# Kernel optimization log

Measured on AMD Instinct MI355X. Metric: run time of the kernel, lower is better.

The kernel has to match this reference:

```python
import jax, jax.numpy as jnp
import numpy as np

D_MODEL = 2048
NUM_HEADS = 16
N_KV_HEADS = 4
HEAD_DIM = D_MODEL // NUM_HEADS  # 128
N_REP = NUM_HEADS // N_KV_HEADS  # 4
WINDOW = 256
ROPE_BASE = 10000.0
B, T = 2, 2048


def setup_inputs() -> dict:
    key = jax.random.key(0)
    ks = jax.random.split(key, 5)
    s_in = 1.0 / np.sqrt(D_MODEL)
    return {
        "x": jax.random.normal(ks[0], (B, T, D_MODEL), jnp.float32),
        "Wq": jax.random.normal(ks[1], (D_MODEL, D_MODEL), jnp.float32) * s_in,
        "Wk": jax.random.normal(ks[2], (D_MODEL, N_KV_HEADS * HEAD_DIM), jnp.float32) * s_in,
        "Wv": jax.random.normal(ks[3], (D_MODEL, N_KV_HEADS * HEAD_DIM), jnp.float32) * s_in,
        "Wo": jax.random.normal(ks[4], (D_MODEL, D_MODEL), jnp.float32) * s_in,
    }


def _rope_tables(seqlen, dtype):
    inv_freq = 1.0 / (ROPE_BASE ** (jnp.arange(0, HEAD_DIM, 2, dtype=jnp.float32) / HEAD_DIM))
    t = jnp.arange(seqlen, dtype=jnp.float32)
    freqs = jnp.outer(t, inv_freq)              # [T, hd/2]
    emb = jnp.concatenate([freqs, freqs], -1)   # [T, hd]
    return jnp.cos(emb).astype(dtype), jnp.sin(emb).astype(dtype)


def _rotate_half(x):
    half = x.shape[-1] // 2
    return jnp.concatenate([-x[..., half:], x[..., :half]], -1)


def reference(x, Wq, Wk, Wv, Wo):
    Bb, Tt, _ = x.shape
    q = (x @ Wq).reshape(Bb, Tt, NUM_HEADS, HEAD_DIM).transpose(0, 2, 1, 3)   # [B,H,T,hd]
    k = (x @ Wk).reshape(Bb, Tt, N_KV_HEADS, HEAD_DIM).transpose(0, 2, 1, 3)  # [B,Hkv,T,hd]
    v = (x @ Wv).reshape(Bb, Tt, N_KV_HEADS, HEAD_DIM).transpose(0, 2, 1, 3)

    cos, sin = _rope_tables(Tt, q.dtype)  # [T, hd] each, broadcast over B,H
    q = q * cos + _rotate_half(q) * sin
    k = k * cos + _rotate_half(k) * sin

    # GQA: repeat kv heads to match query heads
    k = jnp.repeat(k, N_REP, axis=1)
    v = jnp.repeat(v, N_REP, axis=1)

    # banded causal sliding-window mask: 0 <= i - j < WINDOW
    rel = jnp.arange(Tt)[:, None] - jnp.arange(Tt)[None, :]
    allowed = (rel >= 0) & (rel < WINDOW)  # [T, T]

    scale = 1.0 / np.sqrt(HEAD_DIM)
    scores = jnp.einsum('bhqd,bhkd->bhqk', q, k) * scale
    scores = jnp.where(allowed, scores, jnp.finfo(scores.dtype).min)
    probs = jax.nn.softmax(scores, axis=-1)
    y = jnp.einsum('bhqk,bhkd->bhqd', probs, v)
    y = y.transpose(0, 2, 1, 3).reshape(Bb, Tt, D_MODEL)
    return y @ Wo
```

## Files before the change

### kernel.cpp

```cpp
#include <hip/hip_runtime.h>
#include <hip/hip_bf16.h>

#define D_MODEL 2048
#define SEQ_T   2048
#define NQH     16
#define NKVH    4
#define HD      128
#define WIN     256
#define BATCH   2
#define ROWS    (BATCH * SEQ_T)
#define L2_10K  13.287712379549449f
#define GK      2048

typedef __attribute__((ext_vector_type(8))) short bf8_t;
typedef __attribute__((ext_vector_type(4))) float f4_t;

__device__ __forceinline__ float bf2f(unsigned short u) {
    union { unsigned int i; float f; } v; v.i = ((unsigned int)u) << 16; return v.f;
}
__device__ __forceinline__ unsigned short f2bf(float f) {
    union { float f; unsigned int i; } v; v.f = f;
    unsigned int x = v.i;
    unsigned int lsb = (x >> 16) & 1u;
    x += 0x7fffu + lsb;
    return (unsigned short)(x >> 16);
}

__device__ __forceinline__ void async_ld16(const unsigned short* g, unsigned short* l) {
    __builtin_amdgcn_global_load_lds(
        (const __attribute__((address_space(1))) unsigned int*)(g),
        (__attribute__((address_space(3))) unsigned int*)(l), 16, 0, 0);
}

__device__ int sniff_is_f32(const unsigned short* p) {
    int sane = 0;
    for (int i = 0; i < 64; ++i) {
        unsigned short u = p[2 * i];
        int e = (u >> 7) & 0xFF;
        sane += (e >= 100 && e <= 140) ? 1 : 0;
    }
    return sane < 32;
}

__global__ __launch_bounds__(256)
void convert_all(const float* __restrict__ x,
                 const float* __restrict__ Wq, const float* __restrict__ Wk,
                 const float* __restrict__ Wv, const float* __restrict__ Wo,
                 unsigned short* __restrict__ xb,
                 unsigned short* __restrict__ Wqkvt, unsigned short* __restrict__ Wot) {
    __shared__ unsigned short Ts[32][36];
    int id = blockIdx.x;
    const int t = threadIdx.x;
    if (id < 4096) {
        int i = (id * 256 + t) * 8;
        float4 a = *(const float4*)(x + i);
        float4 b = *(const float4*)(x + i + 4);
        ushort4 o0, o1;
        o0.x = f2bf(a.x); o0.y = f2bf(a.y); o0.z = f2bf(a.z); o0.w = f2bf(a.w);
        o1.x = f2bf(b.x); o1.y = f2bf(b.y); o1.z = f2bf(b.z); o1.w = f2bf(b.w);
        *(ushort4*)(xb + i)     = o0;
        *(ushort4*)(xb + i + 4) = o1;
        return;
    }
    id -= 4096;
    const float* W; unsigned short* Wt; int N;
    const int K = D_MODEL;
    if (id < 4096)      { W = Wq; Wt = Wqkvt;                          N = 2048; }
    else if (id < 5120) { W = Wk; Wt = Wqkvt + (size_t)2048 * D_MODEL; N = 512;  id -= 4096; }
    else if (id < 6144) { W = Wv; Wt = Wqkvt + (size_t)2560 * D_MODEL; N = 512;  id -= 5120; }
    else                { W = Wo; Wt = Wot;                            N = 2048; id -= 6144; }
    const int ntn = N >> 5;
    const int n0 = (id % ntn) * 32;
    const int k0 = (id / ntn) * 32;
    {
        int r = t >> 3, c = (t & 7) * 4;
        float4 v = *(const float4*)(W + (size_t)(k0 + r) * N + n0 + c);
        Ts[r][c + 0] = f2bf(v.x); Ts[r][c + 1] = f2bf(v.y);
        Ts[r][c + 2] = f2bf(v.z); Ts[r][c + 3] = f2bf(v.w);
    }
    __syncthreads();
    {
        int n = t >> 3, k = (t & 7) * 4;
        ushort4 o;
        o.x = Ts[k + 0][n]; o.y = Ts[k + 1][n];
        o.z = Ts[k + 2][n]; o.w = Ts[k + 3][n];
        *(ushort4*)(Wt + (size_t)(n0 + n) * K + k0 + k) = o;
    }
}

__global__ __launch_bounds__(256, 3)
void gemm128r(const unsigned short* __restrict__ A,
              const unsigned short* __restrict__ Bt,
              void* __restrict__ Cq, void* __restrict__ Ck, void* __restrict__ Cvc,
              int N, int mode) {
    __shared__ __align__(16) unsigned short Ls[3][8192];

    const int tid  = threadIdx.x;
    const int w    = tid >> 6;
    const int lane = tid & 63;
    const int quad = lane >> 4;
    const int lr   = lane & 15;
    const int wm   = w >> 1;
    const int wn   = w & 1;
    const int sl   = ((quad + (lr >> 1)) & 3) * 8;

    const int ntn = N >> 7;
    const int g   = blockIdx.x;
    const int xcd = g & 7;
    const int r   = g >> 3;
    const int bm  = (xcd & 3) * 8 + (r & 7);
    const int bn  = (xcd >> 2) * (ntn >> 1) + (r >> 3);
    const int m0  = bm * 128;
    const int n0  = bn * 128;

    const unsigned short* srcA[2];
    const unsigned short* srcB[2];
    int dchunk[2];
    #pragma unroll
    for (int l = 0; l < 2; ++l) {
        int li   = l * 256 + tid;
        int row  = li >> 2;
        int slog = ((li & 3) - ((li >> 3) & 3)) & 3;
        srcA[l]   = A  + (size_t)(m0 + row) * GK + slog * 8;
        srcB[l]   = Bt + (size_t)(n0 + row) * GK + slog * 8;
        dchunk[l] = (l * 256 + w * 64) * 8;
    }

    f4_t acc[4][4];
    #pragma unroll
    for (int i = 0; i < 4; ++i)
        #pragma unroll
        for (int j = 0; j < 4; ++j) acc[i][j] = (f4_t){0.f, 0.f, 0.f, 0.f};

#define STAGE(S, KT) do {                                           \
        const int ko_ = (KT) * 32;                                  \
        async_ld16(srcA[0] + ko_, &Ls[S][dchunk[0]]);               \
        async_ld16(srcA[1] + ko_, &Ls[S][dchunk[1]]);               \
        async_ld16(srcB[0] + ko_, &Ls[S][4096 + dchunk[0]]);        \
        async_ld16(srcB[1] + ko_, &Ls[S][4096 + dchunk[1]]);        \
    } while (0)

#define GATE(NN) asm volatile("s_waitcnt vmcnt(" #NN ")" ::: "memory")

    STAGE(0, 0); STAGE(1, 1);
    GATE(4);
    __builtin_amdgcn_s_barrier();

    int Sc = 0, Ss = 2;
    for (int t = 0; t < 64; ++t) {
        const unsigned short* LA = &Ls[Sc][0];
        const unsigned short* LB = &Ls[Sc][4096];
        bf8_t af[4], bv[4];
        #pragma unroll
        for (int mf = 0; mf < 4; ++mf)
            af[mf] = *(const bf8_t*)&LA[(wm * 64 + mf * 16 + lr) * 32 + sl];
        #pragma unroll
        for (int nf = 0; nf < 4; ++nf)
            bv[nf] = *(const bf8_t*)&LB[(wn * 16 + nf * 32 + lr) * 32 + sl];
        if (t < 62) STAGE(Ss, t + 2);
        __builtin_amdgcn_s_setprio(1);
        #pragma unroll
        for (int nf = 0; nf < 4; ++nf)
            #pragma unroll
            for (int mf = 0; mf < 4; ++mf)
                acc[mf][nf] = __builtin_amdgcn_mfma_f32_16x16x32_bf16(
                    af[mf], bv[nf], acc[mf][nf], 0, 0, 0);
        __builtin_amdgcn_s_setprio(0);
        if (t < 62)       GATE(4);
        else if (t == 62) GATE(0);
        if (t < 63) __builtin_amdgcn_s_barrier();
        Sc = (Sc == 2) ? 0 : Sc + 1;
        Ss = (Ss == 2) ? 0 : Ss + 1;
    }

#undef STAGE
#undef GATE

    if (mode == 1) {
        float* C = (float*)Cq;
        #pragma unroll
        for (int mf = 0; mf < 4; ++mf)
            #pragma unroll
            for (int nf = 0; nf < 4; ++nf) {
                int c  = n0 + wn * 16 + nf * 32 + lr;
                int rb = m0 + wm * 64 + mf * 16 + quad * 4;
                #pragma unroll
                for (int rr = 0; rr < 4; ++rr)
                    C[(size_t)(rb + rr) * N + c] = acc[mf][nf][rr];
            }
        return;
    }
    if (n0 < 2048 + 512) {
        const bool isQ = (n0 < 2048);
        unsigned short* Cb = isQ ? (unsigned short*)Cq : (unsigned short*)Ck;
        const int ldc = isQ ? D_MODEL : (NKVH * HD);
        const int cb0 = isQ ? n0 : (n0 - 2048);
        float inv[2];
        #pragma unroll
        for (int p = 0; p < 2; ++p)
            inv[p] = exp2f(-(float)(wn * 16 + p * 32 + lr) * (L2_10K / 64.0f));
        #pragma unroll
        for (int mf = 0; mf < 4; ++mf) {
            #pragma unroll
            for (int rr = 0; rr < 4; ++rr) {
                int row = m0 + wm * 64 + mf * 16 + quad * 4 + rr;
                float tp = (float)(row & (SEQ_T - 1));
                #pragma unroll
                for (int p = 0; p < 2; ++p) {
                    float sn, cs;
                    sincosf(tp * inv[p], &sn, &cs);
                    float lo = acc[mf][p][rr], hi = acc[mf][p + 2][rr];
                    size_t base = (size_t)row * ldc + cb0 + wn * 16 + p * 32 + lr;
                    Cb[base]      = f2bf(lo * cs - hi * sn);
                    Cb[base + 64] = f2bf(hi * cs + lo * sn);
                }
            }
        }
    } else {
        unsigned short* Vc = (unsigned short*)Cvc;
        #pragma unroll
        for (int mf = 0; mf < 4; ++mf)
            #pragma unroll
            for (int nf = 0; nf < 4; ++nf) {
                int n    = (n0 - 2560) + wn * 16 + nf * 32 + lr;
                int kvh2 = n >> 7, d = n & 127;
                int row0 = m0 + wm * 64 + mf * 16 + quad * 4;
                int bb   = row0 >> 11, pos = row0 & (SEQ_T - 1);
                ushort4 o;
                o.x = f2bf(acc[mf][nf][0]); o.y = f2bf(acc[mf][nf][1]);
                o.z = f2bf(acc[mf][nf][2]); o.w = f2bf(acc[mf][nf][3]);
                *(ushort4*)(Vc + (size_t)(bb * 4 + kvh2) * (SEQ_T * HD)
                              + (size_t)(pos >> 5) * 4096 + d * 32 + (pos & 31)) = o;
            }
    }
}

__global__ __launch_bounds__(512, 2)
void gemm128(const unsigned short* __restrict__ A,
             const unsigned short* __restrict__ Bt,
             float* __restrict__ C, int N) {
    __shared__ __align__(16) unsigned short Ls[4][12288];

    const int tid  = threadIdx.x;
    const int w    = tid >> 6;
    const int lane = tid & 63;
    const int quad = lane >> 4;
    const int lr   = lane & 15;
    const int wm   = w >> 2;
    const int wn   = w & 3;
    const int sl   = ((quad + (lr >> 1)) & 3) * 8;

    const int ntn = N >> 8;
    const int g   = blockIdx.x;
    const int xcd = g & 7;
    const int r   = g >> 3;
    const int bm  = (xcd & 3) * 8 + (r & 7);
    const int bn  = (xcd >> 2) * (ntn >> 1) + (r >> 3);
    const int m0  = bm * 128;
    const int n0  = bn * 256;

    const int slog = ((tid & 3) - ((tid >> 3) & 3)) & 3;
    const unsigned short* srcA0 = A  + (size_t)(m0 + (tid >> 2)) * GK + slog * 8;
    const unsigned short* srcB0 = Bt + (size_t)(n0 + (tid >> 2)) * GK + slog * 8;
    const unsigned short* srcB1 = Bt + (size_t)(n0 + 128 + (tid >> 2)) * GK + slog * 8;
    const int dch = w * 512;

    f4_t acc[4][4];
    #pragma unroll
    for (int i = 0; i < 4; ++i)
        #pragma unroll
        for (int j = 0; j < 4; ++j) acc[i][j] = (f4_t){0.f, 0.f, 0.f, 0.f};

#define STAGEB(S, KT) do {                                          \
        const int ko_ = (KT) * 32;                                  \
        async_ld16(srcA0 + ko_, &Ls[S][dch]);                       \
        async_ld16(srcB0 + ko_, &Ls[S][4096 + dch]);                \
        async_ld16(srcB1 + ko_, &Ls[S][8192 + dch]);                \
    } while (0)

#define GATE(NN) asm volatile("s_waitcnt vmcnt(" #NN ")" ::: "memory")

    STAGEB(0, 0); STAGEB(1, 1); STAGEB(2, 2);
    GATE(6);
    __builtin_amdgcn_s_barrier();

    bf8_t af[4], bv[4];
    for (int t = 0; t < 64; ++t) {
        const int S = t & 3;
        #pragma unroll
        for (int mf = 0; mf < 4; ++mf)
            af[mf] = *(const bf8_t*)&Ls[S][(wm * 64 + mf * 16 + lr) * 32 + sl];
        #pragma unroll
        for (int nf = 0; nf < 4; ++nf)
            bv[nf] = *(const bf8_t*)&Ls[S][4096 + (wn * 16 + nf * 64 + lr) * 32 + sl];
        if (t < 61) STAGEB((t + 3) & 3, t + 3);
        __builtin_amdgcn_s_barrier();
        __builtin_amdgcn_s_setprio(1);
        #pragma unroll
        for (int nf = 0; nf < 4; ++nf)
            #pragma unroll
            for (int mf = 0; mf < 4; ++mf)
                acc[mf][nf] = __builtin_amdgcn_mfma_f32_16x16x32_bf16(
                    af[mf], bv[nf], acc[mf][nf], 0, 0, 0);
        __builtin_amdgcn_s_setprio(0);
        if (t < 61)      GATE(6);
        else if (t == 61) GATE(3);
        else if (t == 62) GATE(0);
        if (t < 63) __builtin_amdgcn_s_barrier();
    }

#undef STAGEB
#undef GATE

    #pragma unroll
    for (int mf = 0; mf < 4; ++mf)
        #pragma unroll
        for (int nf = 0; nf < 4; ++nf) {
            int c  = n0 + wn * 16 + nf * 64 + lr;
            int rb = m0 + wm * 64 + mf * 16 + quad * 4;
            #pragma unroll
            for (int rr = 0; rr < 4; ++rr)
                C[(size_t)(rb + rr) * N + c] = acc[mf][nf][rr];
        }
}

__global__ __launch_bounds__(256)
void gemm_dual(const void* __restrict__ A, const void* __restrict__ B,
               void* __restrict__ C, int M, int N, int Kd,
               const unsigned short* __restrict__ sniffp,
               int a_dyn, int c_dyn, int c_trans) {
    __shared__ unsigned short As[64][32];
    __shared__ unsigned short Bs[64][32];
    __shared__ int s_f32;

    const int t = threadIdx.x;
    if (t == 0) s_f32 = sniff_is_f32(sniffp);

    const int m0 = blockIdx.y * 64, n0 = blockIdx.x * 64;
    const int w = t >> 6, lane = t & 63;
    const int wm = w >> 1, wn = w & 1;
    const int quad = lane >> 4, lr = lane & 15;

    f4_t acc[2][2];
    #pragma unroll
    for (int i = 0; i < 2; ++i)
        #pragma unroll
        for (int j = 0; j < 2; ++j)
            acc[i][j] = (f4_t){0.f, 0.f, 0.f, 0.f};

    const int ar = t >> 2, ac = (t & 3) * 8;
    const int bk = t >> 3, bn = (t & 7) * 8;

    __syncthreads();
    const bool in_f32 = (s_f32 != 0);
    const bool a_f32  = in_f32 && (a_dyn != 0);
    const bool c_f32  = in_f32 && (c_dyn != 0);

    for (int k0 = 0; k0 < Kd; k0 += 32) {
        __syncthreads();
        if (a_f32) {
            const float* Af = (const float*)A;
            const float4* pa = (const float4*)(Af + (size_t)(m0 + ar) * Kd + k0 + ac);
            float4 a0 = pa[0], a1 = pa[1];
            unsigned short* d = &As[ar][ac];
            d[0] = f2bf(a0.x); d[1] = f2bf(a0.y); d[2] = f2bf(a0.z); d[3] = f2bf(a0.w);
            d[4] = f2bf(a1.x); d[5] = f2bf(a1.y); d[6] = f2bf(a1.z); d[7] = f2bf(a1.w);
        } else {
            const unsigned short* Au = (const unsigned short*)A;
            *(uint4*)(&As[ar][ac]) = *(const uint4*)(Au + (size_t)(m0 + ar) * Kd + k0 + ac);
        }
        if (in_f32) {
            const float* Bf = (const float*)B;
            const float4* pb = (const float4*)(Bf + (size_t)(k0 + bk) * N + n0 + bn);
            float4 b0 = pb[0], b1 = pb[1];
            Bs[bn + 0][bk] = f2bf(b0.x); Bs[bn + 1][bk] = f2bf(b0.y);
            Bs[bn + 2][bk] = f2bf(b0.z); Bs[bn + 3][bk] = f2bf(b0.w);
            Bs[bn + 4][bk] = f2bf(b1.x); Bs[bn + 5][bk] = f2bf(b1.y);
            Bs[bn + 6][bk] = f2bf(b1.z); Bs[bn + 7][bk] = f2bf(b1.w);
        } else {
            const unsigned short* Bu = (const unsigned short*)B;
            uint4 bv = *(const uint4*)(Bu + (size_t)(k0 + bk) * N + n0 + bn);
            union { uint4 v; unsigned short s[8]; } bu; bu.v = bv;
            #pragma unroll
            for (int j = 0; j < 8; ++j) Bs[bn + j][bk] = bu.s[j];
        }
        __syncthreads();

        bf8_t va0 = *(const bf8_t*)&As[wm * 32 + 0  + lr][quad * 8];
        bf8_t va1 = *(const bf8_t*)&As[wm * 32 + 16 + lr][quad * 8];
        bf8_t vb0 = *(const bf8_t*)&Bs[wn * 32 + 0  + lr][quad * 8];
        bf8_t vb1 = *(const bf8_t*)&Bs[wn * 32 + 16 + lr][quad * 8];

        acc[0][0] = __builtin_amdgcn_mfma_f32_16x16x32_bf16(va0, vb0, acc[0][0], 0, 0, 0);
        acc[0][1] = __builtin_amdgcn_mfma_f32_16x16x32_bf16(va0, vb1, acc[0][1], 0, 0, 0);
        acc[1][0] = __builtin_amdgcn_mfma_f32_16x16x32_bf16(va1, vb0, acc[1][0], 0, 0, 0);
        acc[1][1] = __builtin_amdgcn_mfma_f32_16x16x32_bf16(va1, vb1, acc[1][1], 0, 0, 0);
    }

    if (c_trans) {
        #pragma unroll
        for (int mi = 0; mi < 2; ++mi)
            #pragma unroll
            for (int ni = 0; ni < 2; ++ni) {
                int row0 = m0 + wm * 32 + mi * 16 + quad * 4;
                int col  = n0 + wn * 32 + ni * 16 + lr;
                int kvh2 = col >> 7, d = col & 127;
                int bb   = row0 >> 11, pos = row0 & (SEQ_T - 1);
                ushort4 v;
                v.x = f2bf(acc[mi][ni][0]); v.y = f2bf(acc[mi][ni][1]);
                v.z = f2bf(acc[mi][ni][2]); v.w = f2bf(acc[mi][ni][3]);
                *(ushort4*)((unsigned short*)C + (size_t)(bb * 4 + kvh2) * (SEQ_T * HD)
                              + (size_t)(pos >> 5) * 4096 + d * 32 + (pos & 31)) = v;
            }
    } else {
        #pragma unroll
        for (int mi = 0; mi < 2; ++mi)
            #pragma unroll
            for (int ni = 0; ni < 2; ++ni)
                #pragma unroll
                for (int r = 0; r < 4; ++r) {
                    int row = m0 + wm * 32 + mi * 16 + quad * 4 + r;
                    int col = n0 + wn * 32 + ni * 16 + lr;
                    if (c_f32) ((float*)C)[(size_t)row * N + col] = acc[mi][ni][r];
                    else ((unsigned short*)C)[(size_t)row * N + col] = f2bf(acc[mi][ni][r]);
                }
    }
}

__global__ __launch_bounds__(64)
void rope_kernel(unsigned short* __restrict__ X, int nheads) {
    const int idx = blockIdx.x;
    const int h   = idx % nheads;
    const int row = idx / nheads;
    const int tpos = row % SEQ_T;
    const int i   = threadIdx.x;

    size_t base = (size_t)row * (nheads * HD) + h * HD;
    float inv = exp2f(-(float)i * (L2_10K / 64.0f));
    float a = (float)tpos * inv;
    float s, c;
    sincosf(a, &s, &c);
    float x0 = bf2f(X[base + i]);
    float x1 = bf2f(X[base + i + 64]);
    X[base + i]      = f2bf(x0 * c - x1 * s);
    X[base + i + 64] = f2bf(x1 * c + x0 * s);
}

#define PS  72

__global__ __launch_bounds__(256)
void attn_gqa(unsigned short* __restrict__ Q,
              const unsigned short* __restrict__ K,
              const unsigned short* __restrict__ Vc) {
    __shared__ unsigned short Ks[64][128];
    __shared__ unsigned short Vs[2][8192];
    __shared__ unsigned short Pw[4][32][PS];

    const int t    = threadIdx.x;
    const int g    = blockIdx.x;
    const int xcd  = g & 7;
    const int b    = xcd >> 2;
    const int kvh  = xcd & 3;
    const int q0   = (g >> 3) * 32;
    const int w    = t >> 6;
    const int lane = t & 63;
    const int quad = lane >> 4;
    const int lr   = lane & 15;
    const int h    = kvh * 4 + w;
    const float scale = 0.08838834764831845f;

    bf8_t qf[2][4];
    #pragma unroll
    for (int mt = 0; mt < 2; ++mt) {
        const unsigned short* qrow =
            Q + (size_t)(b * SEQ_T + q0 + mt * 16 + lr) * D_MODEL + h * HD;
        #pragma unroll
        for (int kk = 0; kk < 4; ++kk)
            qf[mt][kk] = *(const bf8_t*)(qrow + kk * 32 + quad * 8);
    }

    f4_t O[2][8];
    #pragma unroll
    for (int mt = 0; mt < 2; ++mt)
        #pragma unroll
        for (int dt = 0; dt < 8; ++dt) O[mt][dt] = (f4_t){0.f, 0.f, 0.f, 0.f};
    float lpart[2][4];
    #pragma unroll
    for (int mt = 0; mt < 2; ++mt)
        #pragma unroll
        for (int r = 0; r < 4; ++r) lpart[mt][r] = 0.f;

    const size_t vbase = (size_t)(b * 4 + kvh) * (SEQ_T * HD);
    const int krow = t >> 2, kcol = (t & 3) * 32;

    const int jstart = (q0 >= 193) ? 0 : ((193 - q0 + 63) >> 6);

    uint4 kreg[4];
    int vb = 0;
    {
        const int kb = q0 - 256 + 64 * jstart;
        int rg = kb + krow;
        rg = rg < 0 ? 0 : (rg > SEQ_T - 1 ? SEQ_T - 1 : rg);
        const unsigned short* src =
            K + (size_t)(b * SEQ_T + rg) * (NKVH * HD) + kvh * HD + kcol;
        #pragma unroll
        for (int i = 0; i < 4; ++i) kreg[i] = *(const uint4*)(src + 8 * i);
        int s0 = kb >> 5;        s0 = s0 < 0 ? 0 : (s0 > 63 ? 63 : s0);
        int s1 = (kb + 32) >> 5; s1 = s1 < 0 ? 0 : (s1 > 63 ? 63 : s1);
        const unsigned short* v0p = Vc + vbase + (size_t)s0 * 4096;
        const unsigned short* v1p = Vc + vbase + (size_t)s1 * 4096;
        #pragma unroll
        for (int i = 0; i < 2; ++i) {
            int off = (w * 2 + i) * 512;
            async_ld16(v0p + off + lane * 8, &Vs[0][off]);
            async_ld16(v1p + off + lane * 8, &Vs[0][4096 + off]);
        }
    }

    for (int j = jstart; j < 5; ++j) {
        const int kb = q0 - 256 + 64 * j;
        const bool need_mask = (j == 0) || (j == 4) || (kb < 0);

        __builtin_amdgcn_s_barrier();
        __builtin_amdgcn_sched_barrier(0);

        #pragma unroll
        for (int i = 0; i < 4; ++i)
            *(uint4*)&Ks[krow][(kcol + 8 * i) ^ ((krow & 7) << 3)] = kreg[i];

        if (j < 4) {
            const int kb2 = kb + 64;
            int rg = kb2 + krow;
            rg = rg < 0 ? 0 : (rg > SEQ_T - 1 ? SEQ_T - 1 : rg);
            const unsigned short* src =
                K + (size_t)(b * SEQ_T + rg) * (NKVH * HD) + kvh * HD + kcol;
            int s0 = kb2 >> 5;        s0 = s0 < 0 ? 0 : (s0 > 63 ? 63 : s0);
            int s1 = (kb2 + 32) >> 5; s1 = s1 < 0 ? 0 : (s1 > 63 ? 63 : s1);
            const unsigned short* v0p = Vc + vbase + (size_t)s0 * 4096;
            const unsigned short* v1p = Vc + vbase + (size_t)s1 * 4096;
            #pragma unroll
            for (int i = 0; i < 2; ++i) {
                int off = (w * 2 + i) * 512;
                async_ld16(v0p + off + lane * 8, &Vs[vb ^ 1][off]);
                async_ld16(v1p + off + lane * 8, &Vs[vb ^ 1][4096 + off]);
            }
            #pragma unroll
            for (int i = 0; i < 4; ++i) kreg[i] = *(const uint4*)(src + 8 * i);
            asm volatile("s_waitcnt vmcnt(8)" ::: "memory");
        } else {
            asm volatile("s_waitcnt vmcnt(0)" ::: "memory");
        }
        asm volatile("s_waitcnt lgkmcnt(0)" ::: "memory");
        __builtin_amdgcn_s_barrier();
        __builtin_amdgcn_sched_barrier(0);

        f4_t s[2][4];
        #pragma unroll
        for (int mt = 0; mt < 2; ++mt)
            #pragma unroll
            for (int nt = 0; nt < 4; ++nt) s[mt][nt] = (f4_t){0.f, 0.f, 0.f, 0.f};
        #pragma unroll
        for (int nt = 0; nt < 4; ++nt) {
            #pragma unroll
            for (int kk = 0; kk < 4; ++kk) {
                bf8_t kf = *(const bf8_t*)&Ks[nt * 16 + lr]
                    [(kk * 32 + quad * 8) ^ ((lr & 7) << 3)];
                s[0][nt] = __builtin_amdgcn_mfma_f32_16x16x32_bf16(qf[0][kk], kf, s[0][nt], 0, 0, 0);
                s[1][nt] = __builtin_amdgcn_mfma_f32_16x16x32_bf16(qf[1][kk], kf, s[1][nt], 0, 0, 0);
            }
        }

        #pragma unroll
        for (int mt = 0; mt < 2; ++mt) {
            #pragma unroll
            for (int r = 0; r < 4; ++r) {
                const int q = q0 + mt * 16 + quad * 4 + r;
                #pragma unroll
                for (int nt = 0; nt < 4; ++nt) {
                    float pj = __expf(s[mt][nt][r] * scale);
                    if (need_mask) {
                        int jg = kb + nt * 16 + lr;
                        bool ok = (jg >= 0) && ((unsigned)(q - jg) < (unsigned)WIN);
                        pj = ok ? pj : 0.f;
                    }
                    lpart[mt][r] += pj;
                    Pw[w][mt * 16 + quad * 4 + r][nt * 16 + lr] = f2bf(pj);
                }
            }
        }

        bf8_t pf[2][2];
        #pragma unroll
        for (int mt = 0; mt < 2; ++mt)
            #pragma unroll
            for (int kk = 0; kk < 2; ++kk)
                pf[mt][kk] = *(const bf8_t*)&Pw[w][mt * 16 + lr][kk * 32 + quad * 8];
        #pragma unroll
        for (int dt = 0; dt < 8; ++dt)
            #pragma unroll
            for (int kk = 0; kk < 2; ++kk) {
                bf8_t vf = *(const bf8_t*)&Vs[vb][kk * 4096 + (dt * 16 + lr) * 32 + quad * 8];
                O[0][dt] = __builtin_amdgcn_mfma_f32_16x16x32_bf16(pf[0][kk], vf, O[0][dt], 0, 0, 0);
                O[1][dt] = __builtin_amdgcn_mfma_f32_16x16x32_bf16(pf[1][kk], vf, O[1][dt], 0, 0, 0);
            }
        vb ^= 1;
    }

    #pragma unroll
    for (int off = 1; off < 16; off <<= 1)
        #pragma unroll
        for (int mt = 0; mt < 2; ++mt)
            #pragma unroll
            for (int r = 0; r < 4; ++r)
                lpart[mt][r] += __shfl_xor(lpart[mt][r], off);

    #pragma unroll
    for (int mt = 0; mt < 2; ++mt) {
        float invl[4];
        #pragma unroll
        for (int r = 0; r < 4; ++r) invl[r] = 1.0f / lpart[mt][r];
        #pragma unroll
        for (int dt = 0; dt < 8; ++dt)
            #pragma unroll
            for (int r = 0; r < 4; ++r)
                Q[(size_t)(b * SEQ_T + q0 + mt * 16 + quad * 4 + r) * D_MODEL
                  + h * HD + dt * 16 + lr] = f2bf(O[mt][dt][r] * invl[r]);
    }
}

extern "C" void kernel_launch(void* const* d_in, const int* in_sizes, int n_in,
                              void* d_out, int out_size, void* d_ws, size_t ws_size,
                              hipStream_t stream) {
    const float* x  = (const float*)d_in[0];
    const float* Wq = (const float*)d_in[1];
    const float* Wk = (const float*)d_in[2];
    const float* Wv = (const float*)d_in[3];
    const float* Wo = (const float*)d_in[4];
    const unsigned short* sniffp = (const unsigned short*)d_in[1];

    unsigned short* Qb  = (unsigned short*)d_ws;
    unsigned short* Kb  = Qb + (size_t)ROWS * D_MODEL;
    unsigned short* Vcb = Kb + (size_t)ROWS * (NKVH * HD);
    unsigned short* Wot = Vcb + (size_t)(NKVH * HD) * ROWS;

    dim3 blk(256);

    if (ws_size >= (size_t)32 * 1024 * 1024) {
        unsigned short* xb    = (unsigned short*)d_out;
        unsigned short* Wqkvt = xb + (size_t)ROWS * D_MODEL;

        convert_all<<<dim3(14336), blk, 0, stream>>>(x, Wq, Wk, Wv, Wo, xb, Wqkvt, Wot);

        gemm128r<<<dim3(768), blk, 0, stream>>>(
            xb, Wqkvt, Qb, Kb, Vcb, D_MODEL + 2 * NKVH * HD, 3);

        attn_gqa<<<dim3(512), blk, 0, stream>>>(Qb, Kb, Vcb);

        gemm128<<<dim3(256), dim3(512), 0, stream>>>(Qb, Wot, (float*)d_out, D_MODEL);
    } else {
        gemm_dual<<<dim3(D_MODEL / 64, ROWS / 64), blk, 0, stream>>>(
            x, Wq, Qb, ROWS, D_MODEL, D_MODEL, sniffp, 1, 0, 0);
        gemm_dual<<<dim3((NKVH * HD) / 64, ROWS / 64), blk, 0, stream>>>(
            x, Wk, Kb, ROWS, NKVH * HD, D_MODEL, sniffp, 1, 0, 0);
        gemm_dual<<<dim3((NKVH * HD) / 64, ROWS / 64), blk, 0, stream>>>(
            x, Wv, Vcb, ROWS, NKVH * HD, D_MODEL, sniffp, 1, 0, 1);
        rope_kernel<<<dim3(ROWS * NQH), dim3(64), 0, stream>>>(Qb, NQH);
        rope_kernel<<<dim3(ROWS * NKVH), dim3(64), 0, stream>>>(Kb, NKVH);
        attn_gqa<<<dim3(512), blk, 0, stream>>>(Qb, Kb, Vcb);
        gemm_dual<<<dim3(D_MODEL / 64, ROWS / 64), blk, 0, stream>>>(
            Qb, Wo, d_out, ROWS, D_MODEL, D_MODEL, sniffp, 0, 1, 0);
    }
}
```

Measured before the change: 252.9 us.

## Split attention into single-wave blocks loading K/V fragments directly from global

Attention now launches one 64-thread block per query head and 32-row tile instead of one 4-wave block per KV head group. The shared K/V staging, double-buffered async loads and block barriers are gone, and each wave loads its K and V MFMA fragments straight from global memory into registers. This removes barrier and LDS round-trip overhead and raises block count, but the four query heads sharing a KV head now each fetch K/V separately. It also loses the prefetch overlap and uses uncoalesced fragment loads that rely on L2 and cache.

```diff
diff --git a/kernel.cpp b/kernel.cpp
--- a/kernel.cpp
+++ b/kernel.cpp
@@ -448,25 +448,22 @@
 
 #define PS  72
 
-__global__ __launch_bounds__(256)
+__global__ __launch_bounds__(64)
 void attn_gqa(unsigned short* __restrict__ Q,
               const unsigned short* __restrict__ K,
               const unsigned short* __restrict__ Vc) {
-    __shared__ unsigned short Ks[64][128];
-    __shared__ unsigned short Vs[2][8192];
-    __shared__ unsigned short Pw[4][32][PS];
+    __shared__ unsigned short Pw[32][PS];
 
     const int t    = threadIdx.x;
     const int g    = blockIdx.x;
     const int xcd  = g & 7;
     const int b    = xcd >> 2;
     const int kvh  = xcd & 3;
-    const int q0   = (g >> 3) * 32;
-    const int w    = t >> 6;
-    const int lane = t & 63;
-    const int quad = lane >> 4;
-    const int lr   = lane & 15;
-    const int h    = kvh * 4 + w;
+    const int h4   = (g >> 3) & 3;
+    const int q0   = (g >> 5) * 32;
+    const int quad = t >> 4;
+    const int lr   = t & 15;
+    const int h    = kvh * 4 + h4;
     const float scale = 0.08838834764831845f;
 
     bf8_t qf[2][4];
@@ -491,87 +488,50 @@
         for (int r = 0; r < 4; ++r) lpart[mt][r] = 0.f;
 
     const size_t vbase = (size_t)(b * 4 + kvh) * (SEQ_T * HD);
-    const int krow = t >> 2, kcol = (t & 3) * 32;
-
     const int jstart = (q0 >= 193) ? 0 : ((193 - q0 + 63) >> 6);
-
-    uint4 kreg[4];
-    int vb = 0;
-    {
-        const int kb = q0 - 256 + 64 * jstart;
-        int rg = kb + krow;
-        rg = rg < 0 ? 0 : (rg > SEQ_T - 1 ? SEQ_T - 1 : rg);
-        const unsigned short* src =
-            K + (size_t)(b * SEQ_T + rg) * (NKVH * HD) + kvh * HD + kcol;
-        #pragma unroll
-        for (int i = 0; i < 4; ++i) kreg[i] = *(const uint4*)(src + 8 * i);
-        int s0 = kb >> 5;        s0 = s0 < 0 ? 0 : (s0 > 63 ? 63 : s0);
-        int s1 = (kb + 32) >> 5; s1 = s1 < 0 ? 0 : (s1 > 63 ? 63 : s1);
-        const unsigned short* v0p = Vc + vbase + (size_t)s0 * 4096;
-        const unsigned short* v1p = Vc + vbase + (size_t)s1 * 4096;
-        #pragma unroll
-        for (int i = 0; i < 2; ++i) {
-            int off = (w * 2 + i) * 512;
-            async_ld16(v0p + off + lane * 8, &Vs[0][off]);
-            async_ld16(v1p + off + lane * 8, &Vs[0][4096 + off]);
-        }
-    }
 
     for (int j = jstart; j < 5; ++j) {
         const int kb = q0 - 256 + 64 * j;
         const bool need_mask = (j == 0) || (j == 4) || (kb < 0);
 
-        __builtin_amdgcn_s_barrier();
-        __builtin_amdgcn_sched_barrier(0);
-
-        #pragma unroll
-        for (int i = 0; i < 4; ++i)
-            *(uint4*)&Ks[krow][(kcol + 8 * i) ^ ((krow & 7) << 3)] = kreg[i];
-
-        if (j < 4) {
-            const int kb2 = kb + 64;
-            int rg = kb2 + krow;
+        bf8_t kf[4][4];
+        #pragma unroll
+        for (int nt = 0; nt < 4; ++nt) {
+            int rg = kb + nt * 16 + lr;
             rg = rg < 0 ? 0 : (rg > SEQ_T - 1 ? SEQ_T - 1 : rg);
-            const unsigned short* src =
-                K + (size_t)(b * SEQ_T + rg) * (NKVH * HD) + kvh * HD + kcol;
-            int s0 = kb2 >> 5;        s0 = s0 < 0 ? 0 : (s0 > 63 ? 63 : s0);
-            int s1 = (kb2 + 32) >> 5; s1 = s1 < 0 ? 0 : (s1 > 63 ? 63 : s1);
-            const unsigned short* v0p = Vc + vbase + (size_t)s0 * 4096;
-            const unsigned short* v1p = Vc + vbase + (size_t)s1 * 4096;
-            #pragma unroll
-            for (int i = 0; i < 2; ++i) {
-                int off = (w * 2 + i) * 512;
-                async_ld16(v0p + off + lane * 8, &Vs[vb ^ 1][off]);
-                async_ld16(v1p + off + lane * 8, &Vs[vb ^ 1][4096 + off]);
+            const unsigned short* kr =
+                K + (size_t)(b * SEQ_T + rg) * (NKVH * HD) + kvh * HD;
+            #pragma unroll
+            for (int kk = 0; kk < 4; ++kk)
+                kf[nt][kk] = *(const bf8_t*)(kr + kk * 32 + quad * 8);
+        }
+
+        f4_t s[2][4];
+        #pragma unroll
+        for (int mt = 0; mt < 2; ++mt)
+            #pragma unroll
+            for (int nt = 0; nt < 4; ++nt) s[mt][nt] = (f4_t){0.f, 0.f, 0.f, 0.f};
+        #pragma unroll
+        for (int nt = 0; nt < 4; ++nt)
+            #pragma unroll
+            for (int kk = 0; kk < 4; ++kk) {
+                s[0][nt] = __builtin_amdgcn_mfma_f32_16x16x32_bf16(qf[0][kk], kf[nt][kk], s[0][nt], 0, 0, 0);
+                s[1][nt] = __builtin_amdgcn_mfma_f32_16x16x32_bf16(qf[1][kk], kf[nt][kk], s[1][nt], 0, 0, 0);
             }
-            #pragma unroll
-            for (int i = 0; i < 4; ++i) kreg[i] = *(const uint4*)(src + 8 * i);
-            asm volatile("s_waitcnt vmcnt(8)" ::: "memory");
-        } else {
-            asm volatile("s_waitcnt vmcnt(0)" ::: "memory");
+
+        bf8_t vf[2][8];
+        #pragma unroll
+        for (int kk = 0; kk < 2; ++kk) {
+            int slb = (kb + kk * 32) >> 5;
+            slb = slb < 0 ? 0 : (slb > 63 ? 63 : slb);
+            const unsigned short* vbp = Vc + vbase + (size_t)slb * 4096 + quad * 8;
+            #pragma unroll
+            for (int dt = 0; dt < 8; ++dt)
+                vf[kk][dt] = *(const bf8_t*)(vbp + (dt * 16 + lr) * 32);
         }
-        asm volatile("s_waitcnt lgkmcnt(0)" ::: "memory");
-        __builtin_amdgcn_s_barrier();
-        __builtin_amdgcn_sched_barrier(0);
-
-        f4_t s[2][4];
+
         #pragma unroll
         for (int mt = 0; mt < 2; ++mt)
-            #pragma unroll
-            for (int nt = 0; nt < 4; ++nt) s[mt][nt] = (f4_t){0.f, 0.f, 0.f, 0.f};
-        #pragma unroll
-        for (int nt = 0; nt < 4; ++nt) {
-            #pragma unroll
-            for (int kk = 0; kk < 4; ++kk) {
-                bf8_t kf = *(const bf8_t*)&Ks[nt * 16 + lr]
-                    [(kk * 32 + quad * 8) ^ ((lr & 7) << 3)];
-                s[0][nt] = __builtin_amdgcn_mfma_f32_16x16x32_bf16(qf[0][kk], kf, s[0][nt], 0, 0, 0);
-                s[1][nt] = __builtin_amdgcn_mfma_f32_16x16x32_bf16(qf[1][kk], kf, s[1][nt], 0, 0, 0);
-            }
-        }
-
-        #pragma unroll
-        for (int mt = 0; mt < 2; ++mt) {
             #pragma unroll
             for (int r = 0; r < 4; ++r) {
                 const int q = q0 + mt * 16 + quad * 4 + r;
@@ -584,26 +544,23 @@
                         pj = ok ? pj : 0.f;
                     }
                     lpart[mt][r] += pj;
-                    Pw[w][mt * 16 + quad * 4 + r][nt * 16 + lr] = f2bf(pj);
+                    Pw[mt * 16 + quad * 4 + r][nt * 16 + lr] = f2bf(pj);
                 }
             }
-        }
 
         bf8_t pf[2][2];
         #pragma unroll
         for (int mt = 0; mt < 2; ++mt)
             #pragma unroll
             for (int kk = 0; kk < 2; ++kk)
-                pf[mt][kk] = *(const bf8_t*)&Pw[w][mt * 16 + lr][kk * 32 + quad * 8];
+                pf[mt][kk] = *(const bf8_t*)&Pw[mt * 16 + lr][kk * 32 + quad * 8];
         #pragma unroll
         for (int dt = 0; dt < 8; ++dt)
             #pragma unroll
             for (int kk = 0; kk < 2; ++kk) {
-                bf8_t vf = *(const bf8_t*)&Vs[vb][kk * 4096 + (dt * 16 + lr) * 32 + quad * 8];
-                O[0][dt] = __builtin_amdgcn_mfma_f32_16x16x32_bf16(pf[0][kk], vf, O[0][dt], 0, 0, 0);
-                O[1][dt] = __builtin_amdgcn_mfma_f32_16x16x32_bf16(pf[1][kk], vf, O[1][dt], 0, 0, 0);
+                O[0][dt] = __builtin_amdgcn_mfma_f32_16x16x32_bf16(pf[0][kk], vf[kk][dt], O[0][dt], 0, 0, 0);
+                O[1][dt] = __builtin_amdgcn_mfma_f32_16x16x32_bf16(pf[1][kk], vf[kk][dt], O[1][dt], 0, 0, 0);
             }
-        vb ^= 1;
     }
 
     #pragma unroll
@@ -654,7 +611,7 @@
         gemm128r<<<dim3(768), blk, 0, stream>>>(
             xb, Wqkvt, Qb, Kb, Vcb, D_MODEL + 2 * NKVH * HD, 3);
 
-        attn_gqa<<<dim3(512), blk, 0, stream>>>(Qb, Kb, Vcb);
+        attn_gqa<<<dim3(2048), dim3(64), 0, stream>>>(Qb, Kb, Vcb);
 
         gemm128<<<dim3(256), dim3(512), 0, stream>>>(Qb, Wot, (float*)d_out, D_MODEL);
     } else {
@@ -666,7 +623,7 @@
             x, Wv, Vcb, ROWS, NKVH * HD, D_MODEL, sniffp, 1, 0, 1);
         rope_kernel<<<dim3(ROWS * NQH), dim3(64), 0, stream>>>(Qb, NQH);
         rope_kernel<<<dim3(ROWS * NKVH), dim3(64), 0, stream>>>(Kb, NKVH);
-        attn_gqa<<<dim3(512), blk, 0, stream>>>(Qb, Kb, Vcb);
+        attn_gqa<<<dim3(2048), dim3(64), 0, stream>>>(Qb, Kb, Vcb);
         gemm_dual<<<dim3(D_MODEL / 64, ROWS / 64), blk, 0, stream>>>(
             Qb, Wo, d_out, ROWS, D_MODEL, D_MODEL, sniffp, 0, 1, 0);
     }
```

Measured after the change: 253.9 us. Within noise of the previous version (+0.4%).
